# Kernel optimization log

Hardware: AMD Instinct MI355X
Metric: run time of the kernel (lower is better)

## Reference

```python
import jax, jax.numpy as jnp
import numpy as np

N_SEG = 128      # number of ragged segments (len(leng))
TOTAL = 32768    # total rows = sum(leng)
D = 1280         # cnn_feature (tf_efficientnet_b0 classifier.in_features)
D_HEAD = 512     # hidden of logits head


def setup_inputs() -> dict:
    key = jax.random.key(0)
    ks = jax.random.split(key, 8)
    # ragged lengths (static at trace time), summing exactly to TOTAL
    rng = np.random.default_rng(0)
    leng = rng.integers(64, 448, size=N_SEG).astype(np.int64)
    leng = np.maximum((leng * (TOTAL / leng.sum())).astype(np.int64), 1)
    leng[-1] += TOTAL - leng.sum()
    segment_ids = jnp.asarray(np.repeat(np.arange(N_SEG), leng), jnp.int32)

    features = jax.random.normal(ks[0], (TOTAL, D), jnp.float32)
    s = 0.02
    Ww = jax.random.normal(ks[1], (D, D), jnp.float32) * s        # proj_w.weight
    bw = jnp.zeros((D,), jnp.float32)                              # proj_w.bias
    v = jax.random.normal(ks[2], (D,), jnp.float32) * s           # proj_v.weight (1,D) squeezed
    W1 = jax.random.normal(ks[3], (D_HEAD, D), jnp.float32) * s   # logits[0].weight
    b1 = jnp.zeros((D_HEAD,), jnp.float32)
    W2 = jax.random.normal(ks[4], (1, D_HEAD), jnp.float32) * s   # logits[3].weight
    b2 = jnp.zeros((1,), jnp.float32)
    return {"features": features, "Ww": Ww, "bw": bw, "v": v,
            "W1": W1, "b1": b1, "W2": W2, "b2": b2,
            "segment_ids": segment_ids}


def reference(features, Ww, bw, v, W1, b1, W2, b2, segment_ids):
    # per-row attention logits: tanh(x @ Ww^T + bw) @ v    -> [TOTAL]
    H = jnp.tanh(features @ Ww.T + bw)
    s = H @ v
    # segment-wise stable softmax (replaces Python loop over leng)
    m = jax.ops.segment_max(s, segment_ids, num_segments=N_SEG)
    e = jnp.exp(s - m[segment_ids])
    z = jax.ops.segment_sum(e, segment_ids, num_segments=N_SEG)
    att = e / z[segment_ids]                                      # [TOTAL]
    # attention-weighted sum pooling per segment -> [N_SEG, D]
    pooled = jax.ops.segment_sum(features * att[:, None], segment_ids,
                                 num_segments=N_SEG)
    # logits head (dropout is identity in eval)
    h = jax.nn.relu(pooled @ W1.T + b1)
    return h @ W2.T + b2                                          # [N_SEG, 1]
```

## Files before the change

kernel.cpp:

```cpp
#include <hip/hip_runtime.h>
#include <hip/hip_bf16.h>


#define TOTAL_ROWS 32768
#define DIM 1280
#define NSEG 128
#define DHEAD 512

typedef _Float16 f16x8 __attribute__((ext_vector_type(8)));
typedef _Float16 f16x4 __attribute__((ext_vector_type(4)));
typedef float f32x4 __attribute__((ext_vector_type(4)));

#define OFF_XH   0
#define OFF_WH   83886080
#define OFF_S    87162880
#define OFF_ATT  87293952
#define OFF_SEG  87425024
#define OFF_POOL 87426048
#define OFF_H    88081408

__device__ __forceinline__ void load_lds16(const void* g, void* l) {
  __builtin_amdgcn_global_load_lds(
      (const __attribute__((address_space(1))) unsigned int*)g,
      (__attribute__((address_space(3))) unsigned int*)l, 16, 0, 0);
}

__device__ __forceinline__ float tanh_fast(float x) {
  float e = __expf(2.0f * x);
  return 1.0f - 2.0f * __builtin_amdgcn_rcpf(e + 1.0f);
}

__global__ void cvt_f16_kernel(const float* __restrict__ a, _Float16* __restrict__ oa,
                               int na8, const float* __restrict__ b,
                               _Float16* __restrict__ ob, int nb8) {
  int i = blockIdx.x * blockDim.x + threadIdx.x;
  const float* in;
  _Float16* out;
  int idx;
  if (i < na8) {
    in = a; out = oa; idx = i;
  } else {
    idx = i - na8;
    if (idx >= nb8) return;
    in = b; out = ob;
  }
  const float4* p = (const float4*)in + (size_t)idx * 2;
  float4 u0 = p[0], u1 = p[1];
  f16x8 h;
  h[0] = (_Float16)u0.x; h[1] = (_Float16)u0.y;
  h[2] = (_Float16)u0.z; h[3] = (_Float16)u0.w;
  h[4] = (_Float16)u1.x; h[5] = (_Float16)u1.y;
  h[6] = (_Float16)u1.z; h[7] = (_Float16)u1.w;
  *((f16x8*)out + idx) = h;
}

__global__ void segstart_kernel(const int* __restrict__ sid,
                                int* __restrict__ segstart, float* __restrict__ s,
                                int total) {
  int i = blockIdx.x * blockDim.x + threadIdx.x;
  if (i >= total) return;
  s[i] = 0.f;
  int sg = sid[i];
  if (i == 0) segstart[0] = 0;
  else if (sid[i - 1] != sg) segstart[sg] = i;
  if (i == total - 1) segstart[sg + 1] = total;
}

__global__ __launch_bounds__(256) void gemm_s_kernel(
    const _Float16* __restrict__ X, const _Float16* __restrict__ W,
    const float* __restrict__ v, const float* __restrict__ bw,
    float* __restrict__ s) {
  __shared__ _Float16 As[128 * 64];
  __shared__ _Float16 Bs[128 * 64];
  const int rowBase = blockIdx.x * 128;
  const int jBase = blockIdx.y * 128;
  const int t = threadIdx.x;
  const int lane = t & 63;
  const int w = t >> 6;
  const int wm = w & 1, wn = w >> 1;
  const int kc = lane >> 4;
  const int lm = lane & 15;

  int aBase[2], bBase[2];
#pragma unroll
  for (int s2 = 0; s2 < 2; ++s2) {
    int swz = ((kc + s2 * 4 + lm) & 7) * 8;
    aBase[s2] = (wm * 64 + lm) * 64 + swz;
    bBase[s2] = (wn * 64 + lm) * 64 + swz;
  }

  const int subrow = lane >> 3;
  const int g = ((lane & 7) - subrow) & 7;
  const _Float16* gA = X + (size_t)(rowBase + w * 32 + subrow) * DIM + g * 8;
  const _Float16* gB = W + (size_t)(jBase + w * 32 + subrow) * DIM + g * 8;

  f32x4 acc[4][4];
  const f32x4 zero = {0.f, 0.f, 0.f, 0.f};
#pragma unroll
  for (int i = 0; i < 4; ++i)
#pragma unroll
    for (int j = 0; j < 4; ++j) acc[i][j] = zero;

  for (int k0 = 0; k0 < DIM; k0 += 64) {
    __syncthreads();
#pragma unroll
    for (int q = 0; q < 4; ++q) {
      load_lds16(gA + k0 + q * (8 * DIM), &As[(w * 256 + q * 64) * 8]);
      load_lds16(gB + k0 + q * (8 * DIM), &Bs[(w * 256 + q * 64) * 8]);
    }
    __syncthreads();

#pragma unroll
    for (int s2 = 0; s2 < 2; ++s2) {
      f16x8 a[4], b[4];
#pragma unroll
      for (int mt = 0; mt < 4; ++mt) {
        a[mt] = *(const f16x8*)&As[aBase[s2] + mt * 1024];
        b[mt] = *(const f16x8*)&Bs[bBase[s2] + mt * 1024];
      }
#pragma unroll
      for (int mt = 0; mt < 4; ++mt)
#pragma unroll
        for (int nt = 0; nt < 4; ++nt)
          acc[mt][nt] = __builtin_amdgcn_mfma_f32_16x16x32_f16(
              a[mt], b[nt], acc[mt][nt], 0, 0, 0);
    }
  }

  const int colBase = jBase + wn * 64 + lm;
  float vv[4], bb[4];
#pragma unroll
  for (int nt = 0; nt < 4; ++nt) {
    int j = colBase + nt * 16;
    vv[nt] = v[j];
    bb[nt] = bw[j];
  }
  const int gq = lane >> 4;
#pragma unroll
  for (int mt = 0; mt < 4; ++mt) {
#pragma unroll
    for (int r = 0; r < 4; ++r) {
      float sumv = 0.f;
#pragma unroll
      for (int nt = 0; nt < 4; ++nt)
        sumv += tanh_fast(acc[mt][nt][r] + bb[nt]) * vv[nt];
      sumv += __shfl_xor(sumv, 1);
      sumv += __shfl_xor(sumv, 2);
      sumv += __shfl_xor(sumv, 4);
      sumv += __shfl_xor(sumv, 8);
      if (lm == 0) {
        int row = rowBase + wm * 64 + mt * 16 + gq * 4 + r;
        atomicAdd(&s[row], sumv);
      }
    }
  }
}

__global__ void softmax_kernel(const float* __restrict__ s,
                               const int* __restrict__ segstart,
                               float* __restrict__ att,
                               float* __restrict__ pooled) {
  int seg = blockIdx.x;
  int st = segstart[seg], en = segstart[seg + 1];
  int t = threadIdx.x;
  for (int c = t; c < DIM; c += 256) pooled[(size_t)seg * DIM + c] = 0.f;
  __shared__ float red[8];
  float m = -1e30f;
  for (int i = st + t; i < en; i += 256) m = fmaxf(m, s[i]);
  for (int d = 1; d < 64; d <<= 1) m = fmaxf(m, __shfl_xor(m, d));
  if ((t & 63) == 0) red[t >> 6] = m;
  __syncthreads();
  m = fmaxf(fmaxf(red[0], red[1]), fmaxf(red[2], red[3]));
  float z = 0.f;
  for (int i = st + t; i < en; i += 256) z += __expf(s[i] - m);
  for (int d = 1; d < 64; d <<= 1) z += __shfl_xor(z, d);
  if ((t & 63) == 0) red[4 + (t >> 6)] = z;
  __syncthreads();
  z = red[4] + red[5] + red[6] + red[7];
  float rz = 1.0f / z;
  for (int i = st + t; i < en; i += 256) att[i] = __expf(s[i] - m) * rz;
}

__global__ void pool_kernel(const _Float16* __restrict__ F,
                            const float* __restrict__ att,
                            const int* __restrict__ segstart,
                            float* __restrict__ pooled) {
  int seg = blockIdx.x, part = blockIdx.y;
  int st = segstart[seg], en = segstart[seg + 1];
  int len = en - st;
  int chunk = (len + 7) >> 3;
  int r0 = st + chunk * part;
  int r1 = min(en, r0 + chunk);
  int t = threadIdx.x;
  float acc[4] = {0.f, 0.f, 0.f, 0.f};
  int r = r0;
  for (; r + 2 <= r1; r += 2) {
    float a0 = att[r], a1 = att[r + 1];
    f16x4 f0 = ((const f16x4*)(F + (size_t)r * DIM))[t];
    f16x4 f1 = ((const f16x4*)(F + (size_t)(r + 1) * DIM))[t];
#pragma unroll
    for (int c = 0; c < 4; ++c) {
      acc[c] = fmaf(a0, (float)f0[c], acc[c]);
      acc[c] = fmaf(a1, (float)f1[c], acc[c]);
    }
  }
  if (r < r1) {
    float a0 = att[r];
    f16x4 f0 = ((const f16x4*)(F + (size_t)r * DIM))[t];
#pragma unroll
    for (int c = 0; c < 4; ++c) acc[c] = fmaf(a0, (float)f0[c], acc[c]);
  }
  float* dst = pooled + (size_t)seg * DIM + t * 4;
#pragma unroll
  for (int c = 0; c < 4; ++c) atomicAdd(dst + c, acc[c]);
}

__global__ void head1_kernel(const float* __restrict__ pooled,
                             const float* __restrict__ W1,
                             const float* __restrict__ b1, float* __restrict__ h) {
  int og = blockIdx.x, sg = blockIdx.y;
  __shared__ float Wt[16 * 65];
  __shared__ float Pt[32 * 65];
  int t = threadIdx.x;
  int tx = t & 15, ty = t >> 4;
  float acc0 = 0.f, acc1 = 0.f;
  for (int kcc = 0; kcc < 20; ++kcc) {
    __syncthreads();
#pragma unroll
    for (int u = 0; u < 4; ++u) {
      int lin = t + 256 * u;
      int o = lin >> 6, kk = lin & 63;
      Wt[o * 65 + kk] = W1[(size_t)(og * 16 + o) * DIM + kcc * 64 + kk];
    }
#pragma unroll
    for (int u = 0; u < 8; ++u) {
      int lin = t + 256 * u;
      int ss = lin >> 6, kk = lin & 63;
      Pt[ss * 65 + kk] = pooled[(size_t)(sg * 32 + ss) * DIM + kcc * 64 + kk];
    }
    __syncthreads();
#pragma unroll
    for (int kk = 0; kk < 64; ++kk) {
      float wv = Wt[tx * 65 + kk];
      acc0 = fmaf(Pt[ty * 65 + kk], wv, acc0);
      acc1 = fmaf(Pt[(ty + 16) * 65 + kk], wv, acc1);
    }
  }
  int o = og * 16 + tx;
  float bias = b1[o];
  h[(size_t)(sg * 32 + ty) * DHEAD + o] = fmaxf(acc0 + bias, 0.f);
  h[(size_t)(sg * 32 + ty + 16) * DHEAD + o] = fmaxf(acc1 + bias, 0.f);
}

__global__ void head2_kernel(const float* __restrict__ h,
                             const float* __restrict__ W2,
                             const float* __restrict__ b2, float* __restrict__ out) {
  int seg = blockIdx.x;
  int t = threadIdx.x;
  float val = h[(size_t)seg * DHEAD + t] * W2[t] +
              h[(size_t)seg * DHEAD + t + 256] * W2[t + 256];
  for (int d = 1; d < 64; d <<= 1) val += __shfl_xor(val, d);
  __shared__ float red[4];
  if ((t & 63) == 0) red[t >> 6] = val;
  __syncthreads();
  if (t == 0) out[seg] = red[0] + red[1] + red[2] + red[3] + b2[0];
}

extern "C" void kernel_launch(void* const* d_in, const int* in_sizes, int n_in,
                              void* d_out, int out_size, void* d_ws, size_t ws_size,
                              hipStream_t stream) {
  const float* features = (const float*)d_in[0];
  const float* Ww = (const float*)d_in[1];
  const float* bw = (const float*)d_in[2];
  const float* v = (const float*)d_in[3];
  const float* W1 = (const float*)d_in[4];
  const float* b1 = (const float*)d_in[5];
  const float* W2 = (const float*)d_in[6];
  const float* b2 = (const float*)d_in[7];
  const int* segids = (const int*)d_in[8];
  float* out = (float*)d_out;

  char* ws = (char*)d_ws;
  _Float16* Xh = (_Float16*)(ws + OFF_XH);
  _Float16* Wh = (_Float16*)(ws + OFF_WH);
  float* s = (float*)(ws + OFF_S);
  float* att = (float*)(ws + OFF_ATT);
  int* segstart = (int*)(ws + OFF_SEG);
  float* pooled = (float*)(ws + OFF_POOL);
  float* h = (float*)(ws + OFF_H);

  const int na8 = TOTAL_ROWS * DIM / 8;
  const int nb8 = DIM * DIM / 8;
  cvt_f16_kernel<<<(na8 + nb8 + 255) / 256, 256, 0, stream>>>(features, Xh, na8,
                                                              Ww, Wh, nb8);
  segstart_kernel<<<TOTAL_ROWS / 256, 256, 0, stream>>>(segids, segstart, s,
                                                        TOTAL_ROWS);

  dim3 ggrid(TOTAL_ROWS / 128, DIM / 128);
  gemm_s_kernel<<<ggrid, 256, 0, stream>>>(Xh, Wh, v, bw, s);

  softmax_kernel<<<NSEG, 256, 0, stream>>>(s, segstart, att, pooled);
  pool_kernel<<<dim3(NSEG, 8), 320, 0, stream>>>(Xh, att, segstart, pooled);
  head1_kernel<<<dim3(32, 4), 256, 0, stream>>>(pooled, W1, b1, h);
  head2_kernel<<<NSEG, 256, 0, stream>>>(h, W2, b2, out);
}
```

Baseline: 476.5 us.

## Fuse segment softmax into pooling and fold init work into convert kernel

Merges the segment-start/zeroing kernel into the fp16 conversion kernel, and fuses the per-segment softmax with the attention-weighted pooling so each pooling block recomputes max and sum over its segment and applies exp on the fly. This removes two kernel launches and the att buffer round trip. In exchange, each of the 8 parts of a segment redundantly recomputes the segment max and sum reductions, and the pooling loop does extra exp work per row.

```diff
diff --git a/kernel.cpp b/kernel.cpp
--- a/kernel.cpp
+++ b/kernel.cpp
@@ -14,7 +14,6 @@
 #define OFF_XH   0
 #define OFF_WH   83886080
 #define OFF_S    87162880
-#define OFF_ATT  87293952
 #define OFF_SEG  87425024
 #define OFF_POOL 87426048
 #define OFF_H    88081408
@@ -30,10 +29,21 @@
   return 1.0f - 2.0f * __builtin_amdgcn_rcpf(e + 1.0f);
 }
 
-__global__ void cvt_f16_kernel(const float* __restrict__ a, _Float16* __restrict__ oa,
-                               int na8, const float* __restrict__ b,
-                               _Float16* __restrict__ ob, int nb8) {
+__global__ void cvt_init_kernel(const float* __restrict__ a, _Float16* __restrict__ oa,
+                                int na8, const float* __restrict__ b,
+                                _Float16* __restrict__ ob, int nb8,
+                                const int* __restrict__ sid,
+                                int* __restrict__ segstart, float* __restrict__ s,
+                                float* __restrict__ pooled) {
   int i = blockIdx.x * blockDim.x + threadIdx.x;
+  if (i < TOTAL_ROWS) {
+    s[i] = 0.f;
+    int sg = sid[i];
+    if (i == 0) segstart[0] = 0;
+    else if (sid[i - 1] != sg) segstart[sg] = i;
+    if (i == TOTAL_ROWS - 1) segstart[sg + 1] = TOTAL_ROWS;
+  }
+  if (i < NSEG * DIM) pooled[i] = 0.f;
   const float* in;
   _Float16* out;
   int idx;
@@ -52,18 +62,6 @@
   h[4] = (_Float16)u1.x; h[5] = (_Float16)u1.y;
   h[6] = (_Float16)u1.z; h[7] = (_Float16)u1.w;
   *((f16x8*)out + idx) = h;
-}
-
-__global__ void segstart_kernel(const int* __restrict__ sid,
-                                int* __restrict__ segstart, float* __restrict__ s,
-                                int total) {
-  int i = blockIdx.x * blockDim.x + threadIdx.x;
-  if (i >= total) return;
-  s[i] = 0.f;
-  int sg = sid[i];
-  if (i == 0) segstart[0] = 0;
-  else if (sid[i - 1] != sg) segstart[sg] = i;
-  if (i == total - 1) segstart[sg + 1] = total;
 }
 
 __global__ __launch_bounds__(256) void gemm_s_kernel(
@@ -156,46 +154,37 @@
   }
 }
 
-__global__ void softmax_kernel(const float* __restrict__ s,
-                               const int* __restrict__ segstart,
-                               float* __restrict__ att,
-                               float* __restrict__ pooled) {
-  int seg = blockIdx.x;
+__global__ void softpool_kernel(const _Float16* __restrict__ F,
+                                const float* __restrict__ s,
+                                const int* __restrict__ segstart,
+                                float* __restrict__ pooled) {
+  int seg = blockIdx.x, part = blockIdx.y;
   int st = segstart[seg], en = segstart[seg + 1];
   int t = threadIdx.x;
-  for (int c = t; c < DIM; c += 256) pooled[(size_t)seg * DIM + c] = 0.f;
-  __shared__ float red[8];
+  __shared__ float redm[5], redz[5];
   float m = -1e30f;
-  for (int i = st + t; i < en; i += 256) m = fmaxf(m, s[i]);
+  for (int i = st + t; i < en; i += 320) m = fmaxf(m, s[i]);
   for (int d = 1; d < 64; d <<= 1) m = fmaxf(m, __shfl_xor(m, d));
-  if ((t & 63) == 0) red[t >> 6] = m;
+  if ((t & 63) == 0) redm[t >> 6] = m;
   __syncthreads();
-  m = fmaxf(fmaxf(red[0], red[1]), fmaxf(red[2], red[3]));
+  m = fmaxf(fmaxf(fmaxf(redm[0], redm[1]), fmaxf(redm[2], redm[3])), redm[4]);
   float z = 0.f;
-  for (int i = st + t; i < en; i += 256) z += __expf(s[i] - m);
+  for (int i = st + t; i < en; i += 320) z += __expf(s[i] - m);
   for (int d = 1; d < 64; d <<= 1) z += __shfl_xor(z, d);
-  if ((t & 63) == 0) red[4 + (t >> 6)] = z;
+  if ((t & 63) == 0) redz[t >> 6] = z;
   __syncthreads();
-  z = red[4] + red[5] + red[6] + red[7];
+  z = redz[0] + redz[1] + redz[2] + redz[3] + redz[4];
   float rz = 1.0f / z;
-  for (int i = st + t; i < en; i += 256) att[i] = __expf(s[i] - m) * rz;
-}
-
-__global__ void pool_kernel(const _Float16* __restrict__ F,
-                            const float* __restrict__ att,
-                            const int* __restrict__ segstart,
-                            float* __restrict__ pooled) {
-  int seg = blockIdx.x, part = blockIdx.y;
-  int st = segstart[seg], en = segstart[seg + 1];
+
   int len = en - st;
   int chunk = (len + 7) >> 3;
   int r0 = st + chunk * part;
   int r1 = min(en, r0 + chunk);
-  int t = threadIdx.x;
   float acc[4] = {0.f, 0.f, 0.f, 0.f};
   int r = r0;
   for (; r + 2 <= r1; r += 2) {
-    float a0 = att[r], a1 = att[r + 1];
+    float a0 = __expf(s[r] - m) * rz;
+    float a1 = __expf(s[r + 1] - m) * rz;
     f16x4 f0 = ((const f16x4*)(F + (size_t)r * DIM))[t];
     f16x4 f1 = ((const f16x4*)(F + (size_t)(r + 1) * DIM))[t];
 #pragma unroll
@@ -205,7 +194,7 @@
     }
   }
   if (r < r1) {
-    float a0 = att[r];
+    float a0 = __expf(s[r] - m) * rz;
     f16x4 f0 = ((const f16x4*)(F + (size_t)r * DIM))[t];
 #pragma unroll
     for (int c = 0; c < 4; ++c) acc[c] = fmaf(a0, (float)f0[c], acc[c]);
@@ -284,23 +273,19 @@
   _Float16* Xh = (_Float16*)(ws + OFF_XH);
   _Float16* Wh = (_Float16*)(ws + OFF_WH);
   float* s = (float*)(ws + OFF_S);
-  float* att = (float*)(ws + OFF_ATT);
   int* segstart = (int*)(ws + OFF_SEG);
   float* pooled = (float*)(ws + OFF_POOL);
   float* h = (float*)(ws + OFF_H);
 
   const int na8 = TOTAL_ROWS * DIM / 8;
   const int nb8 = DIM * DIM / 8;
-  cvt_f16_kernel<<<(na8 + nb8 + 255) / 256, 256, 0, stream>>>(features, Xh, na8,
-                                                              Ww, Wh, nb8);
-  segstart_kernel<<<TOTAL_ROWS / 256, 256, 0, stream>>>(segids, segstart, s,
-                                                        TOTAL_ROWS);
+  cvt_init_kernel<<<(na8 + nb8 + 255) / 256, 256, 0, stream>>>(
+      features, Xh, na8, Ww, Wh, nb8, segids, segstart, s, pooled);
 
   dim3 ggrid(TOTAL_ROWS / 128, DIM / 128);
   gemm_s_kernel<<<ggrid, 256, 0, stream>>>(Xh, Wh, v, bw, s);
 
-  softmax_kernel<<<NSEG, 256, 0, stream>>>(s, segstart, att, pooled);
-  pool_kernel<<<dim3(NSEG, 8), 320, 0, stream>>>(Xh, att, segstart, pooled);
+  softpool_kernel<<<dim3(NSEG, 8), 320, 0, stream>>>(Xh, s, segstart, pooled);
   head1_kernel<<<dim3(32, 4), 256, 0, stream>>>(pooled, W1, b1, h);
   head2_kernel<<<NSEG, 256, 0, stream>>>(h, W2, b2, out);
 }
```

Result: no change. 474.3 us (-0.5%).
